# Kernel tuning notes

Measured on AMD Instinct MI355X. Metric: run time of the kernel, lower is better.

## Reference

```python
import jax, jax.numpy as jnp
import numpy as np

B, T, C, H, K = 16, 8192, 256, 256, 7


def setup_inputs() -> dict:
    key = jax.random.key(0)
    ks = jax.random.split(key, 6)
    x = jax.random.normal(ks[0], (B, T, C), dtype=jnp.float32)
    # ragged lengths in [T//2, T]; padding_mask: True = padding (at tail)
    lengths = jax.random.randint(ks[1], (B,), T // 2, T + 1)
    padding_mask = jnp.arange(T)[None, :] >= lengths[:, None]
    w1 = jax.random.normal(ks[2], (H, C, K), dtype=jnp.float32) / np.sqrt(C * K)
    b1 = jnp.zeros((H,), jnp.float32)
    w2 = jax.random.normal(ks[3], (H, H, 3), dtype=jnp.float32) / np.sqrt(H * 3)
    b2 = jnp.zeros((H,), jnp.float32)
    w3 = jax.random.normal(ks[4], (2, H, 1), dtype=jnp.float32) / np.sqrt(H)
    b3 = jnp.zeros((2,), jnp.float32)
    return {"x": x, "padding_mask": padding_mask,
            "w1": w1, "b1": b1, "w2": w2, "b2": b2, "w3": w3, "b3": b3}


def _conv1d(h, w, b, pad):
    # h: (B, Cin, T), w: (Cout, Cin, K) torch OIW layout
    y = jax.lax.conv_general_dilated(h, w, (1,), [(pad, pad)],
                                     dimension_numbers=("NCH", "OIH", "NCH"))
    return y + b[None, :, None]


def _boundary_logits(x, w1, b1, w2, b2, w3, b3):
    # RebornSegmenter.forward (dropout is identity in eval)
    h = jnp.transpose(x, (0, 2, 1))            # (B, C, T)
    h = jax.nn.relu(_conv1d(h, w1, b1, K // 2))
    h = jax.nn.relu(_conv1d(h, w2, b2, 1))
    h = _conv1d(h, w3, b3, 0)                  # (B, 2, T)
    return jnp.transpose(h, (0, 2, 1))         # (B, T, 2)


def _segment_pool(xb, sid):
    # xb: (T, C), sid: (T,) in [0, T] (T == dropped/padding)
    sums = jax.ops.segment_sum(xb, sid, num_segments=T)
    cnt = jax.ops.segment_sum(jnp.ones((T,), xb.dtype), sid, num_segments=T)
    return sums, cnt


def reference(x, padding_mask, w1, b1, w2, b2, w3, b3):
    # pre_segment with deterministic=True (boundary = argmax of conv logits)
    boundary_logits = _boundary_logits(x, w1, b1, w2, b2, w3, b3)
    boundary = jnp.argmax(boundary_logits, axis=-1)            # (B, T)
    is_b = (boundary == 1) & (~padding_mask)
    # token t belongs to segment = number of boundaries in [0..t]
    seg_id = jnp.cumsum(is_b.astype(jnp.int32), axis=1)
    seg_id = jnp.where(padding_mask, T, seg_id)  # out-of-range -> dropped
    sums, cnt = jax.vmap(_segment_pool)(x, seg_id)             # (B,T,C),(B,T)
    # segment mean; empty segments -> 0 (output padded to T segments, jit-safe;
    # torch crops to max segment count, extra columns here are flagged padded)
    new_logits = jnp.where(cnt[..., None] > 0,
                           sums / jnp.maximum(cnt, 1.0)[..., None], 0.0)
    nb = jnp.sum(is_b, axis=1)
    n_valid = jnp.where(jnp.any(~padding_mask, axis=1), nb + 1, 0)
    new_pad = jnp.arange(T)[None, :] >= n_valid[:, None]       # (B, T)
    return new_logits, new_pad
```

## Files before the change

kernel.cpp:

```cpp
#include <hip/hip_runtime.h>
#include <cstdint>
#include <cstddef>

#define BSZ 16
#define T   8192
#define CDIM 256
#define HDIM 256
#define KW  7

constexpr int BT = BSZ * T;
constexpr float TAU = 2e-3f;
constexpr int RCAP = 8192;

typedef __attribute__((ext_vector_type(8))) short short8;
typedef _Float16 half8 __attribute__((ext_vector_type(8)));
typedef __attribute__((ext_vector_type(4))) float f32x4;

constexpr size_t B_W1T  = 0;
constexpr size_t B_W2T  = B_W1T + 1835008;
constexpr size_t B_V    = B_W2T + 786432;
constexpr size_t B_D    = B_V + 1024;
constexpr size_t B_ISB  = B_D + 524288;
constexpr size_t B_SID  = B_ISB + 524288;
constexpr size_t B_SST  = B_SID + 524288;
constexpr size_t B_SEN  = B_SST + 524288;
constexpr size_t B_NV   = B_SEN + 524288;
constexpr size_t B_UCT  = B_NV + 64;
constexpr size_t B_UL   = B_UCT + 16;
constexpr size_t B_ZERO = B_UL + 32768;
constexpr size_t B_W1B  = B_ZERO + 256;
constexpr size_t B_W2B  = B_W1B + 917504;
constexpr size_t B_H1F  = B_W2B + 393216;
constexpr size_t B_DSUM = B_H1F + 25165824;

__device__ __forceinline__ void gl_lds16(const void* g, void* l) {
    __builtin_amdgcn_global_load_lds(
        (const __attribute__((address_space(1))) unsigned int*)g,
        (__attribute__((address_space(3))) unsigned int*)l,
        16, 0, 0);
}

__device__ __forceinline__ unsigned short f16_rne(float f) {
    _Float16 h = (_Float16)f;
    return __builtin_bit_cast(unsigned short, h);
}


__global__ void repack_kernel(const float* __restrict__ w1, const float* __restrict__ w2,
                              const float* __restrict__ w3,
                              float* __restrict__ W1R, float* __restrict__ W2R,
                              float* __restrict__ v,
                              unsigned short* __restrict__ W1bL, unsigned short* __restrict__ W2bL)
{
    int idx = blockIdx.x * blockDim.x + threadIdx.x;
    int stride = gridDim.x * blockDim.x;
    for (int i = idx; i < HDIM * 1792; i += stride) {
        int h = i / 1792, kc = i % 1792, kw = kc >> 8, c = kc & 255;
        W1R[i] = w1[(size_t)h * 1792 + c * 7 + kw];
    }
    for (int i = idx; i < HDIM * 768; i += stride) {
        int h = i / 768, kc = i % 768, kw = kc >> 8, c = kc & 255;
        W2R[i] = w2[(size_t)h * 768 + c * 3 + kw];
    }
    for (int o = idx; o < 2 * 8 * 28 * 1024; o += stride) {
        int e = o & 7, lane = (o >> 3) & 63, half = (o >> 9) & 1;
        int su = o >> 10;
        int slot = su % 28, rest = su / 28;
        int cc = rest & 7, h0g = rest >> 3;
        int kw = slot >> 2, bq = slot & 3;
        int h = h0g * 128 + half * 64 + lane;
        int c = cc * 32 + bq * 8 + e;
        W1bL[o] = f16_rne(w1[(size_t)h * 1792 + c * 7 + kw]);
    }
    for (int o = idx; o < 2 * 8 * 12 * 1024; o += stride) {
        int e = o & 7, lane = (o >> 3) & 63, half = (o >> 9) & 1;
        int su = o >> 10;
        int slot = su % 12, rest = su / 12;
        int cc = rest & 7, h0g = rest >> 3;
        int kw = slot >> 2, bq = slot & 3;
        int h = h0g * 128 + half * 64 + lane;
        int c = cc * 32 + bq * 8 + e;
        W2bL[o] = f16_rne(w2[(size_t)h * 768 + c * 3 + kw]);
    }
    if (idx < HDIM) v[idx] = w3[HDIM + idx] - w3[idx];
}

__global__ __launch_bounds__(256) void xcast_kernel(const float* __restrict__ x,
                                                    unsigned short* __restrict__ xt)
{
    int j = blockIdx.x * 256 + threadIdx.x;
    int rin = j & 255, wid = (j >> 8) & 3, cc = (j >> 10) & 7, grp = (j >> 13) & 31, b = j >> 18;
    int t = grp * 256 + rin;
    int c0 = cc * 32 + wid * 8;
    const float* src = x + ((size_t)(b * T + t)) * 256 + c0;
    float4 a = *(const float4*)src;
    float4 bb = *(const float4*)(src + 4);
    short8 o;
    o[0] = (short)f16_rne(a.x); o[1] = (short)f16_rne(a.y);
    o[2] = (short)f16_rne(a.z); o[3] = (short)f16_rne(a.w);
    o[4] = (short)f16_rne(bb.x); o[5] = (short)f16_rne(bb.y);
    o[6] = (short)f16_rne(bb.z); o[7] = (short)f16_rne(bb.w);
    *(short8*)(xt + (size_t)j * 8) = o;
}

__device__ __forceinline__ void c1_stageA(const unsigned short* xt, const unsigned short* zerobuf,
                                          half8* Ab, int b, int t0, int cc, int lane, int wid)
{
    #pragma unroll
    for (int part = 0; part < 5; ++part) {
        int row = part * 64 + lane;
        int t = t0 + row - 3;
        const unsigned short* src = zerobuf;
        if (row < 262 && t >= 0 && t < T) {
            int grp = t >> 8, rin = t & 255;
            src = xt + ((size_t)((((b * 32 + grp) * 8 + cc) * 4 + wid) * 256 + rin)) * 8;
        }
        gl_lds16(src, &Ab[wid * 322 + part * 64]);
    }
}
__device__ __forceinline__ void c1_stageB(const unsigned short* WbL, half8* Bb,
                                          int h0g8, int cc, int lane, int wid)
{
    #pragma unroll
    for (int s = 0; s < 14; ++s) {
        int bs = wid * 14 + s;
        int slot = bs >> 1, half = bs & 1;
        const unsigned short* src = WbL
            + ((size_t)(((h0g8 + cc) * 28 + slot) * 2 + half)) * 512 + lane * 8;
        gl_lds16(src, &Bb[slot * 130 + half * 64]);
    }
}

__global__ __launch_bounds__(256) void conv1_mfma(
    const unsigned short* __restrict__ xt,
    const unsigned short* __restrict__ WbL,
    const float* __restrict__ b1,
    const unsigned short* __restrict__ zerobuf,
    unsigned short* __restrict__ h1t)
{
    __shared__ half8 A8[2][4 * 322];
    __shared__ half8 B8[2][28 * 130];
    const int tid = threadIdx.x, lane = tid & 63, wid = tid >> 6;
    const int b  = blockIdx.x >> 5;
    const int grp = blockIdx.x & 31;
    const int t0 = grp << 8;
    const int h0 = blockIdx.y << 7;
    const int h0g8 = blockIdx.y * 8;
    const int q = lane >> 4, l15 = lane & 15;

    f32x4 acc[4][8] = {};

    c1_stageA(xt, zerobuf, A8[0], b, t0, 0, lane, wid);
    c1_stageB(WbL, B8[0], h0g8, 0, lane, wid);

    for (int cc = 0; cc < 8; ++cc) {
        const int cur = cc & 1;
        __syncthreads();
        if (cc < 7) {
            c1_stageA(xt, zerobuf, A8[cur ^ 1], b, t0, cc + 1, lane, wid);
            c1_stageB(WbL, B8[cur ^ 1], h0g8, cc + 1, lane, wid);
        }
        #pragma unroll
        for (int kw = 0; kw < 7; ++kw) {
            half8 ah[4], bh[8];
            const int rbase = wid * 64 + l15 + kw;
            #pragma unroll
            for (int i = 0; i < 4; ++i) ah[i] = A8[cur][q * 322 + rbase + i * 16];
            #pragma unroll
            for (int j = 0; j < 8; ++j) bh[j] = B8[cur][(kw * 4 + q) * 130 + j * 16 + l15];
            #pragma unroll
            for (int i = 0; i < 4; ++i)
                #pragma unroll
                for (int j = 0; j < 8; ++j)
                    acc[i][j] = __builtin_amdgcn_mfma_f32_16x16x32_f16(ah[i], bh[j], acc[i][j], 0, 0, 0);
        }
    }
    #pragma unroll
    for (int j = 0; j < 8; ++j) {
        int h = h0 + j * 16 + l15;
        float bb = b1[h];
        int hcc = h >> 5, hwid = (h >> 3) & 3, he = h & 7;
        size_t hbase = ((size_t)(((b * 32 + grp) * 8 + hcc) * 4 + hwid)) * 2048 + he;
        #pragma unroll
        for (int i = 0; i < 4; ++i) {
            int rb = wid * 64 + i * 16 + q * 4;
            #pragma unroll
            for (int r = 0; r < 4; ++r)
                h1t[hbase + (size_t)(rb + r) * 8] = f16_rne(fmaxf(acc[i][j][r] + bb, 0.f));
        }
    }
}

__device__ __forceinline__ void c2_stageA(const unsigned short* ht, const unsigned short* zerobuf,
                                          half8* Ab, int b, int t0, int cc, int lane, int wid)
{
    #pragma unroll
    for (int part = 0; part < 5; ++part) {
        int row = part * 64 + lane;
        int t = t0 + row - 1;
        const unsigned short* src = zerobuf;
        if (row < 258 && t >= 0 && t < T) {
            int grp = t >> 8, rin = t & 255;
            src = ht + ((size_t)((((b * 32 + grp) * 8 + cc) * 4 + wid) * 256 + rin)) * 8;
        }
        gl_lds16(src, &Ab[wid * 322 + part * 64]);
    }
}
__device__ __forceinline__ void c2_stageB(const unsigned short* WbL, half8* Bb,
                                          int h0g8, int cc, int lane, int wid)
{
    #pragma unroll
    for (int s = 0; s < 6; ++s) {
        int bs = wid * 6 + s;
        int slot = bs >> 1, half = bs & 1;
        const unsigned short* src = WbL
            + ((size_t)(((h0g8 + cc) * 12 + slot) * 2 + half)) * 512 + lane * 8;
        gl_lds16(src, &Bb[slot * 130 + half * 64]);
    }
}

__global__ __launch_bounds__(256) void conv2_mfma(
    const unsigned short* __restrict__ h1t,
    const unsigned short* __restrict__ WbL,
    const float* __restrict__ b2, const float* __restrict__ v,
    const unsigned short* __restrict__ zerobuf,
    float* __restrict__ dlog)
{
    __shared__ half8 A8[2][4 * 322];
    __shared__ half8 B8[2][12 * 130];
    const int tid = threadIdx.x, lane = tid & 63, wid = tid >> 6;
    const int b  = blockIdx.x >> 5;
    const int t0 = (blockIdx.x & 31) << 8;
    const int h0 = blockIdx.y << 7;
    const int h0g8 = blockIdx.y * 8;
    const int q = lane >> 4, l15 = lane & 15;

    f32x4 acc[4][8] = {};

    c2_stageA(h1t, zerobuf, A8[0], b, t0, 0, lane, wid);
    c2_stageB(WbL, B8[0], h0g8, 0, lane, wid);

    for (int cc = 0; cc < 8; ++cc) {
        const int cur = cc & 1;
        __syncthreads();
        if (cc < 7) {
            c2_stageA(h1t, zerobuf, A8[cur ^ 1], b, t0, cc + 1, lane, wid);
            c2_stageB(WbL, B8[cur ^ 1], h0g8, cc + 1, lane, wid);
        }
        #pragma unroll
        for (int kw = 0; kw < 3; ++kw) {
            half8 ah[4], bh[8];
            const int rbase = wid * 64 + l15 + kw;
            #pragma unroll
            for (int i = 0; i < 4; ++i) ah[i] = A8[cur][q * 322 + rbase + i * 16];
            #pragma unroll
            for (int j = 0; j < 8; ++j) bh[j] = B8[cur][(kw * 4 + q) * 130 + j * 16 + l15];
            #pragma unroll
            for (int i = 0; i < 4; ++i)
                #pragma unroll
                for (int j = 0; j < 8; ++j)
                    acc[i][j] = __builtin_amdgcn_mfma_f32_16x16x32_f16(ah[i], bh[j], acc[i][j], 0, 0, 0);
        }
    }
    float vv[8], bb[8];
    #pragma unroll
    for (int j = 0; j < 8; ++j) {
        int h = h0 + j * 16 + l15;
        vv[j] = v[h]; bb[j] = b2[h];
    }
    #pragma unroll
    for (int i = 0; i < 4; ++i) {
        int tb = t0 + wid * 64 + i * 16 + q * 4;
        #pragma unroll
        for (int r = 0; r < 4; ++r) {
            float s = 0.f;
            #pragma unroll
            for (int j = 0; j < 8; ++j)
                s += fmaxf(acc[i][j][r] + bb[j], 0.f) * vv[j];
            #pragma unroll
            for (int m = 1; m < 16; m <<= 1)
                s += __shfl_xor(s, m, 64);
            if (l15 == 0) atomicAdd(&dlog[b * T + tb + r], s);
        }
    }
}

__global__ void boundary_kernel(const float* __restrict__ d, const int* __restrict__ padmask,
                                const float* __restrict__ b3,
                                int* __restrict__ isb, int* __restrict__ ucount,
                                int* __restrict__ ulist)
{
    int bt = blockIdx.x * 256 + threadIdx.x;
    if (bt >= BT) return;
    int pad = padmask[bt];
    float dd = d[bt] + (b3[1] - b3[0]);
    isb[bt] = (pad == 0 && dd > 0.f) ? 1 : 0;
    if (pad == 0 && fabsf(dd) < TAU) {
        int slot = atomicAdd(ucount, 1);
        if (slot < RCAP) ulist[slot] = bt;
    }
}

__global__ __launch_bounds__(256) void recheck_h1(
    const float* __restrict__ x, const float* __restrict__ W1R,
    const float* __restrict__ b1, const float* __restrict__ zerof,
    const int* __restrict__ ulist, const int* __restrict__ ucount,
    float* __restrict__ h1f)
{
    __shared__ float xs[9 * CDIM];
    int n = *ucount; if (n > RCAP) n = RCAP;
    const int tid = threadIdx.x, lane = tid & 63, wid = tid >> 6;
    const int g = tid >> 4, l = tid & 15;
    const int nit = 4 * n;
    for (int item = blockIdx.x; item < nit; item += gridDim.x) {
        const int li = item >> 2, hc = item & 3;
        const int bt = ulist[li];
        const int b = bt >> 13, t = bt & (T - 1);
        __syncthreads();
        for (int r = wid; r < 9; r += 4) {
            int tt = t + r - 4;
            const float* src = (tt >= 0 && tt < T)
                ? x + (size_t)(b * T + tt) * CDIM + lane * 4 : zerof;
            gl_lds16(src, &xs[r * CDIM]);
        }
        __syncthreads();
        #pragma unroll
        for (int s = 0; s < 4; ++s) {
            const int h = hc * 64 + s * 16 + g;
            const float* wr = &W1R[(size_t)h * 1792];
            double p0 = 0.0, p1 = 0.0, p2 = 0.0;
            #pragma unroll 7
            for (int it = 0; it < 28; ++it) {
                const int e = it * 64 + l * 4;
                float4 w4 = *(const float4*)&wr[e];
                double w0 = (double)w4.x, w1v = (double)w4.y,
                       w2v = (double)w4.z, w3v = (double)w4.w;
                const float* x0 = &xs[e];
                p0 += w0 * (double)x0[0] + w1v * (double)x0[1]
                    + w2v * (double)x0[2] + w3v * (double)x0[3];
                const float* x1 = &xs[256 + e];
                p1 += w0 * (double)x1[0] + w1v * (double)x1[1]
                    + w2v * (double)x1[2] + w3v * (double)x1[3];
                const float* x2 = &xs[512 + e];
                p2 += w0 * (double)x2[0] + w1v * (double)x2[1]
                    + w2v * (double)x2[2] + w3v * (double)x2[3];
            }
            #pragma unroll
            for (int m = 1; m < 16; m <<= 1) {
                p0 += __shfl_xor(p0, m);
                p1 += __shfl_xor(p1, m);
                p2 += __shfl_xor(p2, m);
            }
            if (l == 0) {
                double bb = (double)b1[h];
                double a0 = bb + p0, a1 = bb + p1, a2 = bb + p2;
                float* o = &h1f[(size_t)li * 768];
                o[0 * 256 + h] = (t - 1 >= 0 && a0 > 0.0) ? (float)a0 : 0.f;
                o[1 * 256 + h] = (a1 > 0.0) ? (float)a1 : 0.f;
                o[2 * 256 + h] = (t + 1 < T && a2 > 0.0) ? (float)a2 : 0.f;
            }
        }
    }
}

__global__ __launch_bounds__(256) void recheck_h2(
    const float* __restrict__ h1f, const float* __restrict__ W2R,
    const float* __restrict__ b2, const float* __restrict__ w3,
    const int* __restrict__ ulist, const int* __restrict__ ucount,
    double* __restrict__ dsum)
{
    __shared__ float hs[768];
    __shared__ double red[64];
    int n = *ucount; if (n > RCAP) n = RCAP;
    const int tid = threadIdx.x, lane = tid & 63, wid = tid >> 6;
    const int g = tid >> 4, l = tid & 15;
    const int nit = 4 * n;
    for (int item = blockIdx.x; item < nit; item += gridDim.x) {
        const int li = item >> 2, hc = item & 3;
        __syncthreads();
        if (wid < 3)
            gl_lds16(h1f + (size_t)li * 768 + wid * 256 + lane * 4, &hs[wid * 256]);
        __syncthreads();
        #pragma unroll
        for (int s = 0; s < 4; ++s) {
            const int h = hc * 64 + s * 16 + g;
            const float* wr = &W2R[(size_t)h * 768];
            double c0 = 0.0;
            #pragma unroll
            for (int it = 0; it < 12; ++it) {
                const int e = it * 64 + l * 4;
                float4 w4 = *(const float4*)&wr[e];
                const float* hv = &hs[e];
                c0 += (double)w4.x * (double)hv[0] + (double)w4.y * (double)hv[1]
                    + (double)w4.z * (double)hv[2] + (double)w4.w * (double)hv[3];
            }
            #pragma unroll
            for (int m = 1; m < 16; m <<= 1) c0 += __shfl_xor(c0, m);
            if (l == 0) {
                double acc2 = (double)b2[h] + c0;
                double h2v = acc2 > 0.0 ? acc2 : 0.0;
                double vd = (double)w3[HDIM + h] - (double)w3[h];
                red[s * 16 + g] = vd * h2v;
            }
        }
        __syncthreads();
        if (tid < 32) red[tid] += red[tid + 32];
        __syncthreads();
        if (tid < 16) red[tid] += red[tid + 16];
        __syncthreads();
        if (tid == 0) {
            double ssum = 0.0;
            #pragma unroll
            for (int i = 0; i < 16; ++i) ssum += red[i];
            atomicAdd(&dsum[li], ssum);
        }
    }
}

__global__ void recheck_final(const double* __restrict__ dsum, const float* __restrict__ b3,
                              const int* __restrict__ ulist, const int* __restrict__ ucount,
                              int* __restrict__ isb)
{
    int n = *ucount; if (n > RCAP) n = RCAP;
    int li = blockIdx.x * 256 + threadIdx.x;
    if (li >= n) return;
    double dd = dsum[li] + ((double)b3[1] - (double)b3[0]);
    isb[ulist[li]] = (dd > 0.0) ? 1 : 0;
}

__global__ __launch_bounds__(1024) void scan_kernel(
    const int* __restrict__ isb, const int* __restrict__ padmask,
    int* __restrict__ sid, int* __restrict__ nvalid)
{
    __shared__ int ssum[1024];
    const int b = blockIdx.x, tid = threadIdx.x;
    const int base = b * T;
    int vals[8]; int s = 0;
    #pragma unroll
    for (int i = 0; i < 8; ++i) { vals[i] = isb[base + tid * 8 + i]; s += vals[i]; }
    ssum[tid] = s;
    __syncthreads();
    for (int off = 1; off < 1024; off <<= 1) {
        int add = (tid >= off) ? ssum[tid - off] : 0;
        __syncthreads();
        ssum[tid] += add;
        __syncthreads();
    }
    int run = ssum[tid] - s;
    #pragma unroll
    for (int i = 0; i < 8; ++i) {
        int t = tid * 8 + i;
        run += vals[i];
        sid[base + t] = (padmask[base + t] != 0) ? T : run;
    }
    if (tid == 1023) {
        int nb = ssum[1023];
        nvalid[b] = (padmask[base] == 0) ? (nb + 1) : 0;
    }
}

__global__ void segbounds_kernel(const int* __restrict__ sid, const int* __restrict__ padmask,
                                 int* __restrict__ sst, int* __restrict__ sen)
{
    int bt = blockIdx.x * 256 + threadIdx.x;
    if (bt >= BT) return;
    if (padmask[bt] != 0) return;
    int t = bt & (T - 1);
    int b = bt >> 13;
    int s = sid[bt];
    if (t == 0) {
        if (s < T) sst[b * T + s] = 0;
    } else if (s != sid[bt - 1]) {
        if (s < T) sst[b * T + s] = t;
    }
    bool last = (t == T - 1) || (padmask[bt + 1] != 0);
    if (s < T && (last || sid[bt + 1] != s)) sen[b * T + s] = t + 1;
}

__global__ __launch_bounds__(256) void pool_kernel(
    const float* __restrict__ x, const int* __restrict__ sst,
    const int* __restrict__ sen, const int* __restrict__ nvalid,
    float* __restrict__ out)
{
    int slot = blockIdx.x * 4 + (threadIdx.x >> 6);
    int lane = threadIdx.x & 63;
    int b = slot >> 13;
    int s = slot & (T - 1);
    int nv = nvalid[b];
    float4 res = make_float4(0.f, 0.f, 0.f, 0.f);
    if (s < nv) {
        int st = sst[slot], en = sen[slot];
        if (st >= 0 && en > st) {
            float4 a = make_float4(0.f, 0.f, 0.f, 0.f);
            const float* xp = &x[(size_t)(b * T + st) * CDIM + lane * 4];
            for (int t = st; t < en; ++t) {
                float4 xv = *(const float4*)xp;
                a.x += xv.x; a.y += xv.y; a.z += xv.z; a.w += xv.w;
                xp += CDIM;
            }
            float inv = 1.f / (float)(en - st);
            res = make_float4(a.x * inv, a.y * inv, a.z * inv, a.w * inv);
        }
    }
    *(float4*)&out[(size_t)slot * CDIM + lane * 4] = res;
    if (lane == 0) out[(size_t)BT * CDIM + slot] = (s < nv) ? 0.f : 1.f;
}

extern "C" void kernel_launch(void* const* d_in, const int* in_sizes, int n_in,
                              void* d_out, int out_size, void* d_ws, size_t ws_size,
                              hipStream_t stream)
{
    const float* x  = (const float*)d_in[0];
    const int* padmask = (const int*)d_in[1];
    const float* w1 = (const float*)d_in[2];
    const float* b1 = (const float*)d_in[3];
    const float* w2 = (const float*)d_in[4];
    const float* b2 = (const float*)d_in[5];
    const float* w3 = (const float*)d_in[6];
    const float* b3 = (const float*)d_in[7];

    char* ws = (char*)d_ws;
    float* W1R = (float*)(ws + B_W1T);
    float* W2R = (float*)(ws + B_W2T);
    float* v   = (float*)(ws + B_V);
    float* dlog = (float*)(ws + B_D);
    int* isb = (int*)(ws + B_ISB);
    int* sid = (int*)(ws + B_SID);
    int* sst = (int*)(ws + B_SST);
    int* sen = (int*)(ws + B_SEN);
    int* nv  = (int*)(ws + B_NV);
    int* uct = (int*)(ws + B_UCT);
    int* ul  = (int*)(ws + B_UL);
    unsigned short* zerobuf = (unsigned short*)(ws + B_ZERO);
    unsigned short* W1bL = (unsigned short*)(ws + B_W1B);
    unsigned short* W2bL = (unsigned short*)(ws + B_W2B);
    float* h1f = (float*)(ws + B_H1F);
    double* dsum = (double*)(ws + B_DSUM);

    float* out = (float*)d_out;
    unsigned short* h1t = (unsigned short*)out;
    unsigned short* xt  = h1t + (size_t)BT * 256;

    hipMemsetAsync(dlog, 0, BT * sizeof(float), stream);
    hipMemsetAsync(sst, 0xFF, BT * sizeof(int), stream);
    hipMemsetAsync(sen, 0xFF, BT * sizeof(int), stream);
    hipMemsetAsync(uct, 0, sizeof(int), stream);
    hipMemsetAsync(zerobuf, 0, 256, stream);
    hipMemsetAsync(dsum, 0, RCAP * sizeof(double), stream);

    repack_kernel<<<1024, 256, 0, stream>>>(w1, w2, w3, W1R, W2R, v, W1bL, W2bL);
    xcast_kernel<<<BT * 256 / (8 * 256), 256, 0, stream>>>(x, xt);
    conv1_mfma<<<dim3(BSZ * (T / 256), HDIM / 128), 256, 0, stream>>>(
        xt, W1bL, b1, zerobuf, h1t);
    conv2_mfma<<<dim3(BSZ * (T / 256), HDIM / 128), 256, 0, stream>>>(
        h1t, W2bL, b2, v, zerobuf, dlog);
    boundary_kernel<<<BT / 256, 256, 0, stream>>>(dlog, padmask, b3, isb, uct, ul);
    recheck_h1<<<4096, 256, 0, stream>>>(x, W1R, b1, (const float*)zerobuf, ul, uct, h1f);
    recheck_h2<<<4096, 256, 0, stream>>>(h1f, W2R, b2, w3, ul, uct, dsum);
    recheck_final<<<RCAP / 256, 256, 0, stream>>>(dsum, b3, ul, uct, isb);
    scan_kernel<<<BSZ, 1024, 0, stream>>>(isb, padmask, sid, nv);
    segbounds_kernel<<<BT / 256, 256, 0, stream>>>(sid, padmask, sst, sen);
    pool_kernel<<<BT / 4, 256, 0, stream>>>(x, sst, sen, nv, out);
}
```

Baseline: 649.3 us.

## Single-buffer LDS in conv MFMA kernels and request two blocks per CU

```diff
diff --git a/kernel.cpp b/kernel.cpp
--- a/kernel.cpp
+++ b/kernel.cpp
@@ -131,15 +131,15 @@
     }
 }
 
-__global__ __launch_bounds__(256) void conv1_mfma(
+__global__ __launch_bounds__(256, 2) void conv1_mfma(
     const unsigned short* __restrict__ xt,
     const unsigned short* __restrict__ WbL,
     const float* __restrict__ b1,
     const unsigned short* __restrict__ zerobuf,
     unsigned short* __restrict__ h1t)
 {
-    __shared__ half8 A8[2][4 * 322];
-    __shared__ half8 B8[2][28 * 130];
+    __shared__ half8 A8[4 * 322];
+    __shared__ half8 B8[28 * 130];
     const int tid = threadIdx.x, lane = tid & 63, wid = tid >> 6;
     const int b  = blockIdx.x >> 5;
     const int grp = blockIdx.x & 31;
@@ -150,24 +150,19 @@
 
     f32x4 acc[4][8] = {};
 
-    c1_stageA(xt, zerobuf, A8[0], b, t0, 0, lane, wid);
-    c1_stageB(WbL, B8[0], h0g8, 0, lane, wid);
-
     for (int cc = 0; cc < 8; ++cc) {
-        const int cur = cc & 1;
-        __syncthreads();
-        if (cc < 7) {
-            c1_stageA(xt, zerobuf, A8[cur ^ 1], b, t0, cc + 1, lane, wid);
-            c1_stageB(WbL, B8[cur ^ 1], h0g8, cc + 1, lane, wid);
-        }
+        __syncthreads();
+        c1_stageA(xt, zerobuf, A8, b, t0, cc, lane, wid);
+        c1_stageB(WbL, B8, h0g8, cc, lane, wid);
+        __syncthreads();
         #pragma unroll
         for (int kw = 0; kw < 7; ++kw) {
             half8 ah[4], bh[8];
             const int rbase = wid * 64 + l15 + kw;
             #pragma unroll
-            for (int i = 0; i < 4; ++i) ah[i] = A8[cur][q * 322 + rbase + i * 16];
-            #pragma unroll
-            for (int j = 0; j < 8; ++j) bh[j] = B8[cur][(kw * 4 + q) * 130 + j * 16 + l15];
+            for (int i = 0; i < 4; ++i) ah[i] = A8[q * 322 + rbase + i * 16];
+            #pragma unroll
+            for (int j = 0; j < 8; ++j) bh[j] = B8[(kw * 4 + q) * 130 + j * 16 + l15];
             #pragma unroll
             for (int i = 0; i < 4; ++i)
                 #pragma unroll
@@ -219,15 +214,15 @@
     }
 }
 
-__global__ __launch_bounds__(256) void conv2_mfma(
+__global__ __launch_bounds__(256, 2) void conv2_mfma(
     const unsigned short* __restrict__ h1t,
     const unsigned short* __restrict__ WbL,
     const float* __restrict__ b2, const float* __restrict__ v,
     const unsigned short* __restrict__ zerobuf,
     float* __restrict__ dlog)
 {
-    __shared__ half8 A8[2][4 * 322];
-    __shared__ half8 B8[2][12 * 130];
+    __shared__ half8 A8[4 * 322];
+    __shared__ half8 B8[12 * 130];
     const int tid = threadIdx.x, lane = tid & 63, wid = tid >> 6;
     const int b  = blockIdx.x >> 5;
     const int t0 = (blockIdx.x & 31) << 8;
@@ -237,24 +232,19 @@
 
     f32x4 acc[4][8] = {};
 
-    c2_stageA(h1t, zerobuf, A8[0], b, t0, 0, lane, wid);
-    c2_stageB(WbL, B8[0], h0g8, 0, lane, wid);
-
     for (int cc = 0; cc < 8; ++cc) {
-        const int cur = cc & 1;
-        __syncthreads();
-        if (cc < 7) {
-            c2_stageA(h1t, zerobuf, A8[cur ^ 1], b, t0, cc + 1, lane, wid);
-            c2_stageB(WbL, B8[cur ^ 1], h0g8, cc + 1, lane, wid);
-        }
+        __syncthreads();
+        c2_stageA(h1t, zerobuf, A8, b, t0, cc, lane, wid);
+        c2_stageB(WbL, B8, h0g8, cc, lane, wid);
+        __syncthreads();
         #pragma unroll
         for (int kw = 0; kw < 3; ++kw) {
             half8 ah[4], bh[8];
             const int rbase = wid * 64 + l15 + kw;
             #pragma unroll
-            for (int i = 0; i < 4; ++i) ah[i] = A8[cur][q * 322 + rbase + i * 16];
-            #pragma unroll
-            for (int j = 0; j < 8; ++j) bh[j] = B8[cur][(kw * 4 + q) * 130 + j * 16 + l15];
+            for (int i = 0; i < 4; ++i) ah[i] = A8[q * 322 + rbase + i * 16];
+            #pragma unroll
+            for (int j = 0; j < 8; ++j) bh[j] = B8[(kw * 4 + q) * 130 + j * 16 + l15];
             #pragma unroll
             for (int i = 0; i < 4; ++i)
                 #pragma unroll
```

Result: faster. 581.0 us (-10.5%).
